# Performance work log

Measured on AMD Instinct MI355X. Metric: run time of the kernel, lower is better.

The kernel has to match this reference:

```python
import jax, jax.numpy as jnp
import numpy as np

N_NODES = 50000
N_EDGES = 800000
D_IN = 128
D_HID = 128
N_CLS = 47


def setup_inputs() -> dict:
    key = jax.random.key(0)
    ks = jax.random.split(key, 10)
    inp = {
        "features": jax.random.normal(ks[0], (N_NODES, D_IN), dtype=jnp.float32),
        "src": jax.random.randint(ks[1], (N_EDGES,), 0, N_NODES),
        "dst": jax.random.randint(ks[2], (N_EDGES,), 0, N_NODES),
        "Wself0": jax.random.normal(ks[3], (D_IN, D_HID), dtype=jnp.float32) / np.sqrt(D_IN),
        "Wneigh0": jax.random.normal(ks[4], (D_IN, D_HID), dtype=jnp.float32) / np.sqrt(D_IN),
        "b0": jnp.zeros((D_HID,), dtype=jnp.float32),
        "Wself1": jax.random.normal(ks[5], (D_HID, D_HID), dtype=jnp.float32) / np.sqrt(D_HID),
        "Wneigh1": jax.random.normal(ks[6], (D_HID, D_HID), dtype=jnp.float32) / np.sqrt(D_HID),
        "b1": jnp.zeros((D_HID,), dtype=jnp.float32),
        "Wself2": jax.random.normal(ks[7], (D_HID, N_CLS), dtype=jnp.float32) / np.sqrt(D_HID),
        "Wneigh2": jax.random.normal(ks[8], (D_HID, N_CLS), dtype=jnp.float32) / np.sqrt(D_HID),
        "b2": jnp.zeros((N_CLS,), dtype=jnp.float32),
    }
    return inp


def reference(features, src, dst, Wself0, Wneigh0, b0, Wself1, Wneigh1, b1, Wself2, Wneigh2, b2):
    # GraphSAGE (DGL SAGEConv, aggregator_type='mean', eval mode so dropout is identity).
    # Per layer: h_neigh[v] = mean_{(u->v) in E} h[u]; out = h @ W_self + h_neigh @ W_neigh + b
    n = features.shape[0]
    # in-degree for mean aggregation (zero-degree nodes get zero neighbor feature)
    deg = jax.ops.segment_sum(jnp.ones(dst.shape, dtype=features.dtype), dst, num_segments=n)
    inv_deg = (1.0 / jnp.maximum(deg, 1.0))[:, None]  # [N,1]

    def sage_layer(h, Ws, Wn, b, act):
        # gather src features per edge, scatter-add into dst, normalize by in-degree
        agg = jax.ops.segment_sum(h[src], dst, num_segments=n) * inv_deg  # [N, d]
        out = h @ Ws + agg @ Wn + b
        return jax.nn.relu(out) if act else out

    h = sage_layer(features, Wself0, Wneigh0, b0, True)
    h = sage_layer(h, Wself1, Wneigh1, b1, True)
    h = sage_layer(h, Wself2, Wneigh2, b2, False)
    return h
```

## Files before the change

### kernel.cpp

```cpp
#include <hip/hip_runtime.h>

#define D 128
#define NCLS 47
#define CAP 64

typedef short short8 __attribute__((ext_vector_type(8)));
typedef float floatx4 __attribute__((ext_vector_type(4)));
typedef unsigned short ushort8 __attribute__((ext_vector_type(8)));

__device__ __forceinline__ float bf16lo(unsigned int u) {
    union { unsigned int i; float f; } c; c.i = u << 16; return c.f;
}
__device__ __forceinline__ float bf16hi(unsigned int u) {
    union { unsigned int i; float f; } c; c.i = u & 0xffff0000u; return c.f;
}
__device__ __forceinline__ unsigned short f2bf(float f) {
    union { float f; unsigned int i; } c; c.f = f;
    unsigned int r = c.i + 0x7fffu + ((c.i >> 16) & 1u);
    return (unsigned short)(r >> 16);
}
__device__ __forceinline__ unsigned int pack2(float x, float y) {
    return (unsigned int)f2bf(x) | ((unsigned int)f2bf(y) << 16);
}

#define FBm 1024
__global__ __launch_bounds__(256) void fill_prep_kernel(
    const int* __restrict__ src, const int* __restrict__ dst,
    int* __restrict__ cnt, unsigned short* __restrict__ csr, int n_edges,
    const float* __restrict__ f, unsigned int* __restrict__ hA, int npairs, int n,
    const float* __restrict__ Ws0, const float* __restrict__ Wn0, unsigned short* __restrict__ Wt0,
    const float* __restrict__ Ws1, const float* __restrict__ Wn1, unsigned short* __restrict__ Wt1,
    const float* __restrict__ Ws2, const float* __restrict__ Wn2, unsigned short* __restrict__ Wt2) {
    if (blockIdx.x < FBm) {
        int cohort = blockIdx.x & 7;
        int cb = blockIdx.x >> 3;
        int nth = (FBm >> 3) * 256;
        int tid = cb * 256 + threadIdx.x;
        int range = (n + 7) >> 3;
        int lo = cohort * range;
        int hi = lo + range;
        if (hi > n) hi = n;
        for (int e = tid; e < n_edges; e += nth) {
            int d = dst[e];
            if (d >= lo && d < hi) {
                int pos = atomicAdd(&cnt[d], 1);
                if (pos < CAP) csr[d * CAP + pos] = (unsigned short)src[e];
            }
        }
        return;
    }
    int tid = (blockIdx.x - FBm) * 256 + threadIdx.x;
    int stride = (gridDim.x - FBm) * 256;
    int total = npairs + 2 * 128 * 256 + 48 * 256;
    for (int gid = tid; gid < total; gid += stride) {
        if (gid < npairs) {
            float2 v = ((const float2*)f)[gid];
            hA[gid] = pack2(v.x, v.y);
            continue;
        }
        int r = gid - npairs;
        if (r < 128 * 256) {
            int nn = r >> 8, k = r & 255;
            float v = (k < 128) ? Ws0[k * 128 + nn] : Wn0[(k - 128) * 128 + nn];
            Wt0[nn * 256 + k] = f2bf(v);
            continue;
        }
        r -= 128 * 256;
        if (r < 128 * 256) {
            int nn = r >> 8, k = r & 255;
            float v = (k < 128) ? Ws1[k * 128 + nn] : Wn1[(k - 128) * 128 + nn];
            Wt1[nn * 256 + k] = f2bf(v);
            continue;
        }
        r -= 128 * 256;
        if (r < 48 * 256) {
            int nn = r >> 8, k = r & 255;
            float v = 0.0f;
            if (nn < NCLS) v = (k < 128) ? Ws2[k * NCLS + nn] : Wn2[(k - 128) * NCLS + nn];
            Wt2[nn * 256 + k] = f2bf(v);
        }
    }
}

__global__ __launch_bounds__(256) void sage_fused_kernel(
    const unsigned int* __restrict__ hin,
    const unsigned short* __restrict__ csr,
    const int* __restrict__ cnt,
    const unsigned short* __restrict__ Wt,
    const float* __restrict__ bias,
    unsigned short* __restrict__ hout,
    float* __restrict__ out,
    int n, int mode) {
    __shared__ unsigned int selfl[16][68];
    __shared__ unsigned int aggl[16][68];

    int wave = threadIdx.x >> 6;
    int lane = threadIdx.x & 63;
    int base = blockIdx.x * 16;

    for (int i = 0; i < 4; ++i) {
        int li = wave * 4 + i;
        int node = base + li;
        if (node < n) {
            int d = cnt[node];
            if (d > CAP) d = CAP;
            const unsigned short* crow = csr + node * CAP;
            float a0x = 0.f, a0y = 0.f, a1x = 0.f, a1y = 0.f;
            float a2x = 0.f, a2y = 0.f, a3x = 0.f, a3y = 0.f;
            int e = 0;
            for (; e + 8 <= d; e += 8) {
                ushort8 s = *(const ushort8*)(crow + e);
                unsigned int u0 = hin[(size_t)s[0] * 64 + lane];
                unsigned int u1 = hin[(size_t)s[1] * 64 + lane];
                unsigned int u2 = hin[(size_t)s[2] * 64 + lane];
                unsigned int u3 = hin[(size_t)s[3] * 64 + lane];
                unsigned int u4 = hin[(size_t)s[4] * 64 + lane];
                unsigned int u5 = hin[(size_t)s[5] * 64 + lane];
                unsigned int u6 = hin[(size_t)s[6] * 64 + lane];
                unsigned int u7 = hin[(size_t)s[7] * 64 + lane];
                a0x += bf16lo(u0); a0y += bf16hi(u0);
                a1x += bf16lo(u1); a1y += bf16hi(u1);
                a2x += bf16lo(u2); a2y += bf16hi(u2);
                a3x += bf16lo(u3); a3y += bf16hi(u3);
                a0x += bf16lo(u4); a0y += bf16hi(u4);
                a1x += bf16lo(u5); a1y += bf16hi(u5);
                a2x += bf16lo(u6); a2y += bf16hi(u6);
                a3x += bf16lo(u7); a3y += bf16hi(u7);
            }
            for (; e < d; ++e) {
                unsigned int u0 = hin[(size_t)crow[e] * 64 + lane];
                a0x += bf16lo(u0); a0y += bf16hi(u0);
            }
            float inv = 1.0f / fmaxf((float)d, 1.0f);
            float rx = ((a0x + a1x) + (a2x + a3x)) * inv;
            float ry = ((a0y + a1y) + (a2y + a3y)) * inv;
            aggl[li][lane] = pack2(rx, ry);
            selfl[li][lane] = hin[(size_t)node * 64 + lane];
        } else {
            aggl[li][lane] = 0u;
            selfl[li][lane] = 0u;
        }
    }
    __syncthreads();

    int m = lane & 15;
    int quad = lane >> 4;
    int t0 = (mode == 2) ? wave : wave * 2;
    int ntt = (mode == 2) ? ((wave < 3) ? 1 : 0) : 2;
    const unsigned short* arow = (const unsigned short*)&selfl[m][0];
    const unsigned short* lrow = (const unsigned short*)&aggl[m][0];

    floatx4 acc[2];
    acc[0] = (floatx4){0.f, 0.f, 0.f, 0.f};
    acc[1] = (floatx4){0.f, 0.f, 0.f, 0.f};

    if (ntt > 0) {
#pragma unroll
        for (int ko = 0; ko < 128; ko += 32) {
            short8 a = *(const short8*)(arow + ko + quad * 8);
            for (int tt = 0; tt < ntt; ++tt) {
                short8 bfr = *(const short8*)(Wt + (size_t)((t0 + tt) * 16 + m) * 256 + ko + quad * 8);
                acc[tt] = __builtin_amdgcn_mfma_f32_16x16x32_bf16(a, bfr, acc[tt], 0, 0, 0);
            }
        }
#pragma unroll
        for (int ko = 0; ko < 128; ko += 32) {
            short8 a = *(const short8*)(lrow + ko + quad * 8);
            for (int tt = 0; tt < ntt; ++tt) {
                short8 bfr = *(const short8*)(Wt + (size_t)((t0 + tt) * 16 + m) * 256 + 128 + ko + quad * 8);
                acc[tt] = __builtin_amdgcn_mfma_f32_16x16x32_bf16(a, bfr, acc[tt], 0, 0, 0);
            }
        }

        if (mode == 1) {
            for (int tt = 0; tt < ntt; ++tt) {
                int nfeat = (t0 + tt) * 16 + m;
                float bb = bias[nfeat];
#pragma unroll
                for (int r = 0; r < 4; ++r) {
                    int node = base + quad * 4 + r;
                    if (node < n) {
                        float v = fmaxf(acc[tt][r] + bb, 0.0f);
                        hout[(size_t)node * 128 + nfeat] = f2bf(v);
                    }
                }
            }
        } else {
            int nfeat = t0 * 16 + m;
            if (nfeat < NCLS) {
                float bb = bias[nfeat];
#pragma unroll
                for (int r = 0; r < 4; ++r) {
                    int node = base + quad * 4 + r;
                    if (node < n) out[(size_t)node * NCLS + nfeat] = acc[0][r] + bb;
                }
            }
        }
    }
}

extern "C" void kernel_launch(void* const* d_in, const int* in_sizes, int n_in,
                              void* d_out, int out_size, void* d_ws, size_t ws_size,
                              hipStream_t stream) {
    const float* features = (const float*)d_in[0];
    const int* src = (const int*)d_in[1];
    const int* dst = (const int*)d_in[2];
    const float* Ws0 = (const float*)d_in[3];
    const float* Wn0 = (const float*)d_in[4];
    const float* b0 = (const float*)d_in[5];
    const float* Ws1 = (const float*)d_in[6];
    const float* Wn1 = (const float*)d_in[7];
    const float* b1 = (const float*)d_in[8];
    const float* Ws2 = (const float*)d_in[9];
    const float* Wn2 = (const float*)d_in[10];
    const float* b2 = (const float*)d_in[11];
    float* out = (float*)d_out;

    int n = in_sizes[0] / D;
    int n_edges = in_sizes[1];

    int* cnt = (int*)d_ws;
    unsigned short* csr = (unsigned short*)(cnt + 50048);
    unsigned int* hA = (unsigned int*)(csr + (size_t)n * CAP + 32);
    unsigned int* hB = hA + (size_t)n * 64;
    unsigned short* Wt0 = (unsigned short*)(hB + (size_t)n * 64);
    unsigned short* Wt1 = Wt0 + 128 * 256;
    unsigned short* Wt2 = Wt1 + 128 * 256;

    int npairs = n * 64;

    hipMemsetAsync(cnt, 0, (size_t)n * sizeof(int), stream);
    fill_prep_kernel<<<2048, 256, 0, stream>>>(
        src, dst, cnt, csr, n_edges, features, hA, npairs, n,
        Ws0, Wn0, Wt0, Ws1, Wn1, Wt1, Ws2, Wn2, Wt2);

    int tiles = (n + 15) / 16;

    sage_fused_kernel<<<tiles, 256, 0, stream>>>(hA, csr, cnt, Wt0, b0,
                                                 (unsigned short*)hB, nullptr, n, 1);
    sage_fused_kernel<<<tiles, 256, 0, stream>>>(hB, csr, cnt, Wt1, b1,
                                                 (unsigned short*)hA, nullptr, n, 1);
    sage_fused_kernel<<<tiles, 256, 0, stream>>>(hA, csr, cnt, Wt2, b2,
                                                 nullptr, out, n, 2);
}
```

Baseline: 332.8 us.

## Build CSR in two passes via 128-node buckets with shared-memory atomics

Edge insertion now runs in two passes. The first pass appends packed (dst,src) records into per-bucket arrays of 128 destination nodes using one global atomic per edge on 391 counters. A second kernel scatters each bucket into the CSR with shared-memory atomics, which replaces the per-node global atomics and their contention. The sage kernel also drops the self-feature LDS staging and reads the A operand straight from global memory. The cost is an extra kernel launch and a pass over the records, and buckets holding more than 2560 edges would silently drop edges.

```diff
diff --git a/kernel.cpp b/kernel.cpp
--- a/kernel.cpp
+++ b/kernel.cpp
@@ -3,6 +3,9 @@
 #define D 128
 #define NCLS 47
 #define CAP 64
+#define BSH 7
+#define NB 391
+#define CAPB 2560
 
 typedef short short8 __attribute__((ext_vector_type(8)));
 typedef float floatx4 __attribute__((ext_vector_type(4)));
@@ -23,34 +26,32 @@
     return (unsigned int)f2bf(x) | ((unsigned int)f2bf(y) << 16);
 }
 
-#define FBm 1024
-__global__ __launch_bounds__(256) void fill_prep_kernel(
+#define SB1 1024
+__global__ __launch_bounds__(256) void fill1_prep_kernel(
     const int* __restrict__ src, const int* __restrict__ dst,
-    int* __restrict__ cnt, unsigned short* __restrict__ csr, int n_edges,
+    int* __restrict__ bcnt, unsigned int* __restrict__ recs, int n_edges,
     const float* __restrict__ f, unsigned int* __restrict__ hA, int npairs, int n,
     const float* __restrict__ Ws0, const float* __restrict__ Wn0, unsigned short* __restrict__ Wt0,
     const float* __restrict__ Ws1, const float* __restrict__ Wn1, unsigned short* __restrict__ Wt1,
     const float* __restrict__ Ws2, const float* __restrict__ Wn2, unsigned short* __restrict__ Wt2) {
-    if (blockIdx.x < FBm) {
+    if (blockIdx.x < SB1) {
         int cohort = blockIdx.x & 7;
         int cb = blockIdx.x >> 3;
-        int nth = (FBm >> 3) * 256;
+        int nth = (SB1 >> 3) * 256;
         int tid = cb * 256 + threadIdx.x;
-        int range = (n + 7) >> 3;
-        int lo = cohort * range;
-        int hi = lo + range;
-        if (hi > n) hi = n;
         for (int e = tid; e < n_edges; e += nth) {
             int d = dst[e];
-            if (d >= lo && d < hi) {
-                int pos = atomicAdd(&cnt[d], 1);
-                if (pos < CAP) csr[d * CAP + pos] = (unsigned short)src[e];
+            int b = d >> BSH;
+            if ((b & 7) == cohort) {
+                int pos = atomicAdd(&bcnt[b], 1);
+                if (pos < CAPB)
+                    recs[(size_t)b * CAPB + pos] = ((unsigned int)d << 16) | (unsigned int)src[e];
             }
         }
         return;
     }
-    int tid = (blockIdx.x - FBm) * 256 + threadIdx.x;
-    int stride = (gridDim.x - FBm) * 256;
+    int tid = (blockIdx.x - SB1) * 256 + threadIdx.x;
+    int stride = (gridDim.x - SB1) * 256;
     int total = npairs + 2 * 128 * 256 + 48 * 256;
     for (int gid = tid; gid < total; gid += stride) {
         if (gid < npairs) {
@@ -79,6 +80,31 @@
             if (nn < NCLS) v = (k < 128) ? Ws2[k * NCLS + nn] : Wn2[(k - 128) * NCLS + nn];
             Wt2[nn * 256 + k] = f2bf(v);
         }
+    }
+}
+
+__global__ __launch_bounds__(256) void csr_build_kernel(
+    const unsigned int* __restrict__ recs, const int* __restrict__ bcnt,
+    unsigned short* __restrict__ csr, int* __restrict__ cnt, int n) {
+    __shared__ int lcnt[128];
+    int b = blockIdx.x;
+    int lo = b << BSH;
+    if (threadIdx.x < 128) lcnt[threadIdx.x] = 0;
+    __syncthreads();
+    int m = bcnt[b];
+    if (m > CAPB) m = CAPB;
+    const unsigned int* rb = recs + (size_t)b * CAPB;
+    for (int i = threadIdx.x; i < m; i += 256) {
+        unsigned int r = rb[i];
+        int d = (int)(r >> 16);
+        int s = (int)(r & 0xFFFFu);
+        int pos = atomicAdd(&lcnt[d - lo], 1);
+        if (pos < CAP) csr[(size_t)d * CAP + pos] = (unsigned short)s;
+    }
+    __syncthreads();
+    if (threadIdx.x < 128) {
+        int node = lo + threadIdx.x;
+        if (node < n) cnt[node] = lcnt[threadIdx.x];
     }
 }
 
@@ -91,7 +117,6 @@
     unsigned short* __restrict__ hout,
     float* __restrict__ out,
     int n, int mode) {
-    __shared__ unsigned int selfl[16][68];
     __shared__ unsigned int aggl[16][68];
 
     int wave = threadIdx.x >> 6;
@@ -104,7 +129,7 @@
         if (node < n) {
             int d = cnt[node];
             if (d > CAP) d = CAP;
-            const unsigned short* crow = csr + node * CAP;
+            const unsigned short* crow = csr + (size_t)node * CAP;
             float a0x = 0.f, a0y = 0.f, a1x = 0.f, a1y = 0.f;
             float a2x = 0.f, a2y = 0.f, a3x = 0.f, a3y = 0.f;
             int e = 0;
@@ -135,10 +160,8 @@
             float rx = ((a0x + a1x) + (a2x + a3x)) * inv;
             float ry = ((a0y + a1y) + (a2y + a3y)) * inv;
             aggl[li][lane] = pack2(rx, ry);
-            selfl[li][lane] = hin[(size_t)node * 64 + lane];
         } else {
             aggl[li][lane] = 0u;
-            selfl[li][lane] = 0u;
         }
     }
     __syncthreads();
@@ -147,7 +170,9 @@
     int quad = lane >> 4;
     int t0 = (mode == 2) ? wave : wave * 2;
     int ntt = (mode == 2) ? ((wave < 3) ? 1 : 0) : 2;
-    const unsigned short* arow = (const unsigned short*)&selfl[m][0];
+    int row_node = base + m;
+    if (row_node >= n) row_node = n - 1;
+    const unsigned short* arow = (const unsigned short*)hin + (size_t)row_node * 128;
     const unsigned short* lrow = (const unsigned short*)&aggl[m][0];
 
     floatx4 acc[2];
@@ -219,7 +244,9 @@
     int n = in_sizes[0] / D;
     int n_edges = in_sizes[1];
 
-    int* cnt = (int*)d_ws;
+    int* bcnt = (int*)d_ws;
+    unsigned int* recs = (unsigned int*)(bcnt + 512);
+    int* cnt = (int*)(recs + (size_t)NB * CAPB);
     unsigned short* csr = (unsigned short*)(cnt + 50048);
     unsigned int* hA = (unsigned int*)(csr + (size_t)n * CAP + 32);
     unsigned int* hB = hA + (size_t)n * 64;
@@ -229,10 +256,11 @@
 
     int npairs = n * 64;
 
-    hipMemsetAsync(cnt, 0, (size_t)n * sizeof(int), stream);
-    fill_prep_kernel<<<2048, 256, 0, stream>>>(
-        src, dst, cnt, csr, n_edges, features, hA, npairs, n,
+    hipMemsetAsync(bcnt, 0, 512 * sizeof(int), stream);
+    fill1_prep_kernel<<<2048, 256, 0, stream>>>(
+        src, dst, bcnt, recs, n_edges, features, hA, npairs, n,
         Ws0, Wn0, Wt0, Ws1, Wn1, Wt1, Ws2, Wn2, Wt2);
+    csr_build_kernel<<<NB, 256, 0, stream>>>(recs, bcnt, csr, cnt, n);
 
     int tiles = (n + 15) / 16;
 
```

Result: slower. 882.8 us (+165.3%).

## Merge all stages into one cooperative persistent kernel with grid syncs

Applied to the files above, without the earlier changes.

Replaces the memset plus four separate launches with a single cooperative mega-kernel that zeroes the counts, builds the CSR, prepares the weights and runs the three SAGE layers, with grid-wide syncs between stages. The fused layer now loops persistently over tiles and reads the self-feature rows straight from global memory instead of staging them in LDS. The aim is to remove launch gaps and tail effects between kernels. In exchange, grid syncs add cost, the persistent grid is capped at 2048 blocks, and the fill cohorts shrink because the grid is split in half.

```diff
diff --git a/kernel.cpp b/kernel.cpp
--- a/kernel.cpp
+++ b/kernel.cpp
@@ -1,4 +1,7 @@
 #include <hip/hip_runtime.h>
+#include <hip/hip_cooperative_groups.h>
+
+namespace cg = cooperative_groups;
 
 #define D 128
 #define NCLS 47
@@ -23,34 +26,41 @@
     return (unsigned int)f2bf(x) | ((unsigned int)f2bf(y) << 16);
 }
 
-#define FBm 1024
-__global__ __launch_bounds__(256) void fill_prep_kernel(
-    const int* __restrict__ src, const int* __restrict__ dst,
-    int* __restrict__ cnt, unsigned short* __restrict__ csr, int n_edges,
-    const float* __restrict__ f, unsigned int* __restrict__ hA, int npairs, int n,
+
+__device__ __forceinline__ void dev_zero(int* __restrict__ cnt, int n) {
+    int tid = blockIdx.x * blockDim.x + threadIdx.x;
+    int stride = gridDim.x * blockDim.x;
+    for (int i = tid; i < n; i += stride) cnt[i] = 0;
+}
+
+__device__ __forceinline__ void dev_fill(const int* __restrict__ src, const int* __restrict__ dst,
+                                         int* __restrict__ cnt, unsigned short* __restrict__ csr,
+                                         int n_edges, int n, int FBk) {
+    int cohort = blockIdx.x & 7;
+    int cb = blockIdx.x >> 3;
+    int nth = (FBk >> 3) * 256;
+    int tid = cb * 256 + threadIdx.x;
+    int range = (n + 7) >> 3;
+    int lo = cohort * range;
+    int hi = lo + range;
+    if (hi > n) hi = n;
+    for (int e = tid; e < n_edges; e += nth) {
+        int d = dst[e];
+        if (d >= lo && d < hi) {
+            int pos = atomicAdd(&cnt[d], 1);
+            if (pos < CAP) csr[(size_t)d * CAP + pos] = (unsigned short)src[e];
+        }
+    }
+}
+
+__device__ __forceinline__ void dev_prep(
+    const float* __restrict__ f, unsigned int* __restrict__ hA, int npairs,
     const float* __restrict__ Ws0, const float* __restrict__ Wn0, unsigned short* __restrict__ Wt0,
     const float* __restrict__ Ws1, const float* __restrict__ Wn1, unsigned short* __restrict__ Wt1,
-    const float* __restrict__ Ws2, const float* __restrict__ Wn2, unsigned short* __restrict__ Wt2) {
-    if (blockIdx.x < FBm) {
-        int cohort = blockIdx.x & 7;
-        int cb = blockIdx.x >> 3;
-        int nth = (FBm >> 3) * 256;
-        int tid = cb * 256 + threadIdx.x;
-        int range = (n + 7) >> 3;
-        int lo = cohort * range;
-        int hi = lo + range;
-        if (hi > n) hi = n;
-        for (int e = tid; e < n_edges; e += nth) {
-            int d = dst[e];
-            if (d >= lo && d < hi) {
-                int pos = atomicAdd(&cnt[d], 1);
-                if (pos < CAP) csr[d * CAP + pos] = (unsigned short)src[e];
-            }
-        }
-        return;
-    }
-    int tid = (blockIdx.x - FBm) * 256 + threadIdx.x;
-    int stride = (gridDim.x - FBm) * 256;
+    const float* __restrict__ Ws2, const float* __restrict__ Wn2, unsigned short* __restrict__ Wt2,
+    int FBk) {
+    int tid = (blockIdx.x - FBk) * 256 + threadIdx.x;
+    int stride = (gridDim.x - FBk) * 256;
     int total = npairs + 2 * 128 * 256 + 48 * 256;
     for (int gid = tid; gid < total; gid += stride) {
         if (gid < npairs) {
@@ -82,121 +92,171 @@
     }
 }
 
-__global__ __launch_bounds__(256) void sage_fused_kernel(
-    const unsigned int* __restrict__ hin,
-    const unsigned short* __restrict__ csr,
-    const int* __restrict__ cnt,
-    const unsigned short* __restrict__ Wt,
-    const float* __restrict__ bias,
-    unsigned short* __restrict__ hout,
-    float* __restrict__ out,
-    int n, int mode) {
-    __shared__ unsigned int selfl[16][68];
+__device__ __forceinline__ void dev_fused(const unsigned int* __restrict__ hin,
+                                          const unsigned short* __restrict__ csr,
+                                          const int* __restrict__ cnt,
+                                          const unsigned short* __restrict__ Wt,
+                                          const float* __restrict__ bias,
+                                          unsigned short* __restrict__ hout,
+                                          float* __restrict__ out,
+                                          int n, int mode) {
     __shared__ unsigned int aggl[16][68];
-
     int wave = threadIdx.x >> 6;
     int lane = threadIdx.x & 63;
-    int base = blockIdx.x * 16;
-
-    for (int i = 0; i < 4; ++i) {
-        int li = wave * 4 + i;
-        int node = base + li;
-        if (node < n) {
-            int d = cnt[node];
-            if (d > CAP) d = CAP;
-            const unsigned short* crow = csr + node * CAP;
-            float a0x = 0.f, a0y = 0.f, a1x = 0.f, a1y = 0.f;
-            float a2x = 0.f, a2y = 0.f, a3x = 0.f, a3y = 0.f;
-            int e = 0;
-            for (; e + 8 <= d; e += 8) {
-                ushort8 s = *(const ushort8*)(crow + e);
-                unsigned int u0 = hin[(size_t)s[0] * 64 + lane];
-                unsigned int u1 = hin[(size_t)s[1] * 64 + lane];
-                unsigned int u2 = hin[(size_t)s[2] * 64 + lane];
-                unsigned int u3 = hin[(size_t)s[3] * 64 + lane];
-                unsigned int u4 = hin[(size_t)s[4] * 64 + lane];
-                unsigned int u5 = hin[(size_t)s[5] * 64 + lane];
-                unsigned int u6 = hin[(size_t)s[6] * 64 + lane];
-                unsigned int u7 = hin[(size_t)s[7] * 64 + lane];
-                a0x += bf16lo(u0); a0y += bf16hi(u0);
-                a1x += bf16lo(u1); a1y += bf16hi(u1);
-                a2x += bf16lo(u2); a2y += bf16hi(u2);
-                a3x += bf16lo(u3); a3y += bf16hi(u3);
-                a0x += bf16lo(u4); a0y += bf16hi(u4);
-                a1x += bf16lo(u5); a1y += bf16hi(u5);
-                a2x += bf16lo(u6); a2y += bf16hi(u6);
-                a3x += bf16lo(u7); a3y += bf16hi(u7);
+    int ntiles = (n + 15) >> 4;
+    for (int tile = blockIdx.x; tile < ntiles; tile += gridDim.x) {
+        int base = tile * 16;
+        for (int i = 0; i < 4; ++i) {
+            int li = wave * 4 + i;
+            int node = base + li;
+            if (node < n) {
+                int d = cnt[node];
+                if (d > CAP) d = CAP;
+                const unsigned short* crow = csr + (size_t)node * CAP;
+                float a0x = 0.f, a0y = 0.f, a1x = 0.f, a1y = 0.f;
+                float a2x = 0.f, a2y = 0.f, a3x = 0.f, a3y = 0.f;
+                int e = 0;
+                for (; e + 8 <= d; e += 8) {
+                    ushort8 s = *(const ushort8*)(crow + e);
+                    unsigned int u0 = hin[(size_t)s[0] * 64 + lane];
+                    unsigned int u1 = hin[(size_t)s[1] * 64 + lane];
+                    unsigned int u2 = hin[(size_t)s[2] * 64 + lane];
+                    unsigned int u3 = hin[(size_t)s[3] * 64 + lane];
+                    unsigned int u4 = hin[(size_t)s[4] * 64 + lane];
+                    unsigned int u5 = hin[(size_t)s[5] * 64 + lane];
+                    unsigned int u6 = hin[(size_t)s[6] * 64 + lane];
+                    unsigned int u7 = hin[(size_t)s[7] * 64 + lane];
+                    a0x += bf16lo(u0); a0y += bf16hi(u0);
+                    a1x += bf16lo(u1); a1y += bf16hi(u1);
+                    a2x += bf16lo(u2); a2y += bf16hi(u2);
+                    a3x += bf16lo(u3); a3y += bf16hi(u3);
+                    a0x += bf16lo(u4); a0y += bf16hi(u4);
+                    a1x += bf16lo(u5); a1y += bf16hi(u5);
+                    a2x += bf16lo(u6); a2y += bf16hi(u6);
+                    a3x += bf16lo(u7); a3y += bf16hi(u7);
+                }
+                for (; e < d; ++e) {
+                    unsigned int u0 = hin[(size_t)crow[e] * 64 + lane];
+                    a0x += bf16lo(u0); a0y += bf16hi(u0);
+                }
+                float inv = 1.0f / fmaxf((float)d, 1.0f);
+                float rx = ((a0x + a1x) + (a2x + a3x)) * inv;
+                float ry = ((a0y + a1y) + (a2y + a3y)) * inv;
+                aggl[li][lane] = pack2(rx, ry);
+            } else {
+                aggl[li][lane] = 0u;
             }
-            for (; e < d; ++e) {
-                unsigned int u0 = hin[(size_t)crow[e] * 64 + lane];
-                a0x += bf16lo(u0); a0y += bf16hi(u0);
+        }
+        __syncthreads();
+
+        int m = lane & 15;
+        int quad = lane >> 4;
+        int t0 = (mode == 2) ? wave : wave * 2;
+        int ntt = (mode == 2) ? ((wave < 3) ? 1 : 0) : 2;
+        int row_node = base + m;
+        if (row_node >= n) row_node = n - 1;
+        const unsigned short* arow = (const unsigned short*)hin + (size_t)row_node * 128;
+        const unsigned short* lrow = (const unsigned short*)&aggl[m][0];
+
+        floatx4 acc[2];
+        acc[0] = (floatx4){0.f, 0.f, 0.f, 0.f};
+        acc[1] = (floatx4){0.f, 0.f, 0.f, 0.f};
+
+        if (ntt > 0) {
+#pragma unroll
+            for (int ko = 0; ko < 128; ko += 32) {
+                short8 a = *(const short8*)(arow + ko + quad * 8);
+                for (int tt = 0; tt < ntt; ++tt) {
+                    short8 bfr = *(const short8*)(Wt + (size_t)((t0 + tt) * 16 + m) * 256 + ko + quad * 8);
+                    acc[tt] = __builtin_amdgcn_mfma_f32_16x16x32_bf16(a, bfr, acc[tt], 0, 0, 0);
+                }
             }
-            float inv = 1.0f / fmaxf((float)d, 1.0f);
-            float rx = ((a0x + a1x) + (a2x + a3x)) * inv;
-            float ry = ((a0y + a1y) + (a2y + a3y)) * inv;
-            aggl[li][lane] = pack2(rx, ry);
-            selfl[li][lane] = hin[(size_t)node * 64 + lane];
-        } else {
-            aggl[li][lane] = 0u;
-            selfl[li][lane] = 0u;
-        }
-    }
-    __syncthreads();
-
-    int m = lane & 15;
-    int quad = lane >> 4;
-    int t0 = (mode == 2) ? wave : wave * 2;
-    int ntt = (mode == 2) ? ((wave < 3) ? 1 : 0) : 2;
-    const unsigned short* arow = (const unsigned short*)&selfl[m][0];
-    const unsigned short* lrow = (const unsigned short*)&aggl[m][0];
-
-    floatx4 acc[2];
-    acc[0] = (floatx4){0.f, 0.f, 0.f, 0.f};
-    acc[1] = (floatx4){0.f, 0.f, 0.f, 0.f};
-
-    if (ntt > 0) {
 #pragma unroll
-        for (int ko = 0; ko < 128; ko += 32) {
-            short8 a = *(const short8*)(arow + ko + quad * 8);
-            for (int tt = 0; tt < ntt; ++tt) {
-                short8 bfr = *(const short8*)(Wt + (size_t)((t0 + tt) * 16 + m) * 256 + ko + quad * 8);
-                acc[tt] = __builtin_amdgcn_mfma_f32_16x16x32_bf16(a, bfr, acc[tt], 0, 0, 0);
+            for (int ko = 0; ko < 128; ko += 32) {
+                short8 a = *(const short8*)(lrow + ko + quad * 8);
+                for (int tt = 0; tt < ntt; ++tt) {
+                    short8 bfr = *(const short8*)(Wt + (size_t)((t0 + tt) * 16 + m) * 256 + 128 + ko + quad * 8);
+                    acc[tt] = __builtin_amdgcn_mfma_f32_16x16x32_bf16(a, bfr, acc[tt], 0, 0, 0);
+                }
             }
-        }
+            if (mode == 1) {
+                for (int tt = 0; tt < ntt; ++tt) {
+                    int nfeat = (t0 + tt) * 16 + m;
+                    float bb = bias[nfeat];
 #pragma unroll
-        for (int ko = 0; ko < 128; ko += 32) {
-            short8 a = *(const short8*)(lrow + ko + quad * 8);
-            for (int tt = 0; tt < ntt; ++tt) {
-                short8 bfr = *(const short8*)(Wt + (size_t)((t0 + tt) * 16 + m) * 256 + 128 + ko + quad * 8);
-                acc[tt] = __builtin_amdgcn_mfma_f32_16x16x32_bf16(a, bfr, acc[tt], 0, 0, 0);
+                    for (int r = 0; r < 4; ++r) {
+                        int node = base + quad * 4 + r;
+                        if (node < n) {
+                            float v = fmaxf(acc[tt][r] + bb, 0.0f);
+                            hout[(size_t)node * 128 + nfeat] = f2bf(v);
+                        }
+                    }
+                }
+            } else {
+                int nfeat = t0 * 16 + m;
+                if (nfeat < NCLS) {
+                    float bb = bias[nfeat];
+#pragma unroll
+                    for (int r = 0; r < 4; ++r) {
+                        int node = base + quad * 4 + r;
+                        if (node < n) out[(size_t)node * NCLS + nfeat] = acc[0][r] + bb;
+                    }
+                }
             }
         }
-
-        if (mode == 1) {
-            for (int tt = 0; tt < ntt; ++tt) {
-                int nfeat = (t0 + tt) * 16 + m;
-                float bb = bias[nfeat];
-#pragma unroll
-                for (int r = 0; r < 4; ++r) {
-                    int node = base + quad * 4 + r;
-                    if (node < n) {
-                        float v = fmaxf(acc[tt][r] + bb, 0.0f);
-                        hout[(size_t)node * 128 + nfeat] = f2bf(v);
-                    }
-                }
-            }
-        } else {
-            int nfeat = t0 * 16 + m;
-            if (nfeat < NCLS) {
-                float bb = bias[nfeat];
-#pragma unroll
-                for (int r = 0; r < 4; ++r) {
-                    int node = base + quad * 4 + r;
-                    if (node < n) out[(size_t)node * NCLS + nfeat] = acc[0][r] + bb;
-                }
-            }
-        }
-    }
+        __syncthreads();
+    }
+}
+
+
+__global__ __launch_bounds__(256) void mega_kernel(
+    const float* f, const int* src, const int* dst,
+    const float* Ws0, const float* Wn0, const float* b0,
+    const float* Ws1, const float* Wn1, const float* b1,
+    const float* Ws2, const float* Wn2, const float* b2,
+    float* out,
+    int* cnt, unsigned short* csr, unsigned int* hA, unsigned int* hB,
+    unsigned short* Wt0, unsigned short* Wt1, unsigned short* Wt2,
+    int n, int n_edges) {
+    cg::grid_group g = cg::this_grid();
+    int npairs = n * 64;
+    int FBk = ((int)gridDim.x >> 1) & ~7;
+
+    dev_zero(cnt, n);
+    g.sync();
+    if ((int)blockIdx.x < FBk)
+        dev_fill(src, dst, cnt, csr, n_edges, n, FBk);
+    else
+        dev_prep(f, hA, npairs, Ws0, Wn0, Wt0, Ws1, Wn1, Wt1, Ws2, Wn2, Wt2, FBk);
+    g.sync();
+    dev_fused(hA, csr, cnt, Wt0, b0, (unsigned short*)hB, nullptr, n, 1);
+    g.sync();
+    dev_fused(hB, csr, cnt, Wt1, b1, (unsigned short*)hA, nullptr, n, 1);
+    g.sync();
+    dev_fused(hA, csr, cnt, Wt2, b2, nullptr, out, n, 2);
+}
+
+
+__global__ void zero_cnt_kernel(int* cnt, int n) { dev_zero(cnt, n); }
+
+__global__ __launch_bounds__(256) void fill_prep_kernel(
+    const int* src, const int* dst, int* cnt, unsigned short* csr, int n_edges,
+    const float* f, unsigned int* hA, int npairs, int n,
+    const float* Ws0, const float* Wn0, unsigned short* Wt0,
+    const float* Ws1, const float* Wn1, unsigned short* Wt1,
+    const float* Ws2, const float* Wn2, unsigned short* Wt2) {
+    const int FBk = 1024;
+    if ((int)blockIdx.x < FBk)
+        dev_fill(src, dst, cnt, csr, n_edges, n, FBk);
+    else
+        dev_prep(f, hA, npairs, Ws0, Wn0, Wt0, Ws1, Wn1, Wt1, Ws2, Wn2, Wt2, FBk);
+}
+
+__global__ __launch_bounds__(256) void sage_fused_kernel(
+    const unsigned int* hin, const unsigned short* csr, const int* cnt,
+    const unsigned short* Wt, const float* bias,
+    unsigned short* hout, float* out, int n, int mode) {
+    dev_fused(hin, csr, cnt, Wt, bias, hout, out, n, mode);
 }
 
 extern "C" void kernel_launch(void* const* d_in, const int* in_sizes, int n_in,
@@ -229,17 +289,39 @@
 
     int npairs = n * 64;
 
-    hipMemsetAsync(cnt, 0, (size_t)n * sizeof(int), stream);
-    fill_prep_kernel<<<2048, 256, 0, stream>>>(
-        src, dst, cnt, csr, n_edges, features, hA, npairs, n,
-        Ws0, Wn0, Wt0, Ws1, Wn1, Wt1, Ws2, Wn2, Wt2);
-
-    int tiles = (n + 15) / 16;
-
-    sage_fused_kernel<<<tiles, 256, 0, stream>>>(hA, csr, cnt, Wt0, b0,
-                                                 (unsigned short*)hB, nullptr, n, 1);
-    sage_fused_kernel<<<tiles, 256, 0, stream>>>(hB, csr, cnt, Wt1, b1,
-                                                 (unsigned short*)hA, nullptr, n, 1);
-    sage_fused_kernel<<<tiles, 256, 0, stream>>>(hA, csr, cnt, Wt2, b2,
-                                                 nullptr, out, n, 2);
-}
+    int nb = 0;
+    hipError_t oerr = hipOccupancyMaxActiveBlocksPerMultiprocessor(
+        &nb, (const void*)mega_kernel, 256, 0);
+    bool coop_ok = false;
+    if (oerr == hipSuccess && nb >= 6) {
+        int G = nb * 256;
+        if (G > 2048) G = 2048;
+        G &= ~7;
+        void* kargs[] = {
+            (void*)&features, (void*)&src, (void*)&dst,
+            (void*)&Ws0, (void*)&Wn0, (void*)&b0,
+            (void*)&Ws1, (void*)&Wn1, (void*)&b1,
+            (void*)&Ws2, (void*)&Wn2, (void*)&b2,
+            (void*)&out,
+            (void*)&cnt, (void*)&csr, (void*)&hA, (void*)&hB,
+            (void*)&Wt0, (void*)&Wt1, (void*)&Wt2,
+            (void*)&n, (void*)&n_edges};
+        hipError_t lerr = hipLaunchCooperativeKernel(
+            (const void*)mega_kernel, dim3(G), dim3(256), kargs, 0, stream);
+        coop_ok = (lerr == hipSuccess);
+    }
+
+    if (!coop_ok) {
+        zero_cnt_kernel<<<(n + 255) / 256, 256, 0, stream>>>(cnt, n);
+        fill_prep_kernel<<<2048, 256, 0, stream>>>(
+            src, dst, cnt, csr, n_edges, features, hA, npairs, n,
+            Ws0, Wn0, Wt0, Ws1, Wn1, Wt1, Ws2, Wn2, Wt2);
+        int tiles = (n + 15) / 16;
+        sage_fused_kernel<<<tiles, 256, 0, stream>>>(hA, csr, cnt, Wt0, b0,
+                                                     (unsigned short*)hB, nullptr, n, 1);
+        sage_fused_kernel<<<tiles, 256, 0, stream>>>(hB, csr, cnt, Wt1, b1,
+                                                     (unsigned short*)hA, nullptr, n, 1);
+        sage_fused_kernel<<<tiles, 256, 0, stream>>>(hA, csr, cnt, Wt2, b2,
+                                                     nullptr, out, n, 2);
+    }
+}
```

Measured after the change: 372.1 us. 1.12x slower.
